# Optimization experiments

Measured on AMD Instinct MI355X. Metric: run time of the kernel, lower is better.

The kernel has to match this reference:

```python
import jax, jax.numpy as jnp
import numpy as np

THRESHOLD = 0.3
NEG_BIG = -2.0 ** 32  # matches tf -2**32 causal mask constant


def setup_inputs() -> dict:
    key = jax.random.key(0)
    kq, kt, kv = jax.random.split(key, 3)
    B, S, D = 16, 2048, 128
    Q = jax.random.normal(kq, (B, S, D), dtype=jnp.float32)
    T = jax.random.normal(kt, (B, S, D), dtype=jnp.float32)
    V = jax.random.normal(kv, (B, S, D), dtype=jnp.float32)
    return {"Q": Q, "T": T, "V": V}


def reference(Q, T, V):
    # scores: [B, S, S]
    A = jnp.einsum('bqd,bkd->bqk', Q, T)
    # Faithful to tf.where(A>thr, A, -2**32 * cast(A>thr)):
    # the false branch evaluates to 0 (mask is 0 there), NOT -2**32.
    A = jnp.where(A > THRESHOLD, A, jnp.zeros((), A.dtype))
    S = Q.shape[1]
    causal = jnp.triu(jnp.ones((S, S), dtype=bool), k=1)  # strictly upper = masked
    A = A + jnp.where(causal, jnp.asarray(NEG_BIG, A.dtype), jnp.zeros((), A.dtype))
    d_k = jnp.asarray(Q.shape[-1], A.dtype)
    A = A / jnp.sqrt(d_k)
    y = jax.nn.softmax(A, axis=-1)
    return jnp.einsum('bqk,bkd->bqd', y, V)
```

## Files before the change

### kernel.cpp

```cpp
#include <hip/hip_runtime.h>
#include <hip/hip_bf16.h>


#define S_LEN 2048
#define D_DIM 128
#define BQ 64
#define BK 64
#define THRESH 0.3f
#define SCALE 0.08838834764831845f

typedef __bf16 bf16x8 __attribute__((ext_vector_type(8)));
typedef float f32x4 __attribute__((ext_vector_type(4)));

__global__ void vt_kernel(const float* __restrict__ V, __bf16* __restrict__ Vt) {
    __shared__ float tile[64][65];
    int bid = blockIdx.x;
    int b  = bid >> 6;
    int t2 = bid & 63;
    int s0 = (t2 >> 1) * 64;
    int d0 = (t2 & 1) * 64;
    int tid = threadIdx.x;
    #pragma unroll
    for (int it = 0; it < 2; ++it) {
        int row = it * 32 + (tid >> 3);
        int c   = (tid & 7) * 8;
        const float* p = V + ((size_t)b * S_LEN + s0 + row) * D_DIM + d0 + c;
        *(f32x4*)(&tile[row][c])     = *(const f32x4*)p;
        *(f32x4*)(&tile[row][c + 4]) = *(const f32x4*)(p + 4);
    }
    __syncthreads();
    #pragma unroll
    for (int it = 0; it < 2; ++it) {
        int dr = it * 32 + (tid >> 3);
        int c  = (tid & 7) * 8;
        bf16x8 w;
        #pragma unroll
        for (int j = 0; j < 8; ++j) w[j] = (__bf16)tile[c + j][dr];
        *(bf16x8*)(Vt + ((size_t)b * D_DIM + d0 + dr) * S_LEN + s0 + c) = w;
    }
}

__global__ __launch_bounds__(256, 2)
void fa_kernel(const float* __restrict__ Q, const float* __restrict__ T,
               const __bf16* __restrict__ Vt, float* __restrict__ O) {
    __shared__ __bf16 Tt[64 * 136];
    __shared__ __bf16 Vl[128 * 72];
    __shared__ __bf16 Pl[4][16 * 72];

    int bid  = blockIdx.x;
    int b    = bid & 15;
    int half = bid >> 8;
    int idx  = (bid >> 4) & 15;
    int qt   = half == 0 ? (31 - idx) : idx;
    int q0   = qt * BQ;

    int tid  = threadIdx.x;
    int lane = tid & 63;
    int wave = tid >> 6;
    int col  = lane & 15;
    int quad = lane >> 4;

    const float* qptr = Q + ((size_t)b * S_LEN + (q0 + wave * 16 + col)) * D_DIM + quad * 8;
    bf16x8 qf[4];
    #pragma unroll
    for (int kk = 0; kk < 4; ++kk) {
        f32x4 a = *(const f32x4*)(qptr + kk * 32);
        f32x4 c = *(const f32x4*)(qptr + kk * 32 + 4);
        #pragma unroll
        for (int j = 0; j < 4; ++j) { qf[kk][j] = (__bf16)a[j]; qf[kk][4 + j] = (__bf16)c[j]; }
    }

    f32x4 oacc[8];
    #pragma unroll
    for (int dt = 0; dt < 8; ++dt) oacc[dt] = {0.f, 0.f, 0.f, 0.f};
    float lsum[4] = {0.f, 0.f, 0.f, 0.f};

    f32x4 tr[8]; bf16x8 vr[4];
    auto loadTiles = [&](int k0) {
        #pragma unroll
        for (int it = 0; it < 4; ++it) {
            int flat = it * 2048 + tid * 8;
            int row = flat >> 7, c = flat & 127;
            const float* p = T + ((size_t)b * S_LEN + k0 + row) * D_DIM + c;
            tr[2 * it]     = *(const f32x4*)p;
            tr[2 * it + 1] = *(const f32x4*)(p + 4);
        }
        #pragma unroll
        for (int it = 0; it < 4; ++it) {
            int flat = it * 2048 + tid * 8;
            int d = flat >> 6, kk2 = flat & 63;
            vr[it] = *(const bf16x8*)(Vt + ((size_t)b * D_DIM + d) * S_LEN + k0 + kk2);
        }
    };
    auto storeTiles = [&]() {
        #pragma unroll
        for (int it = 0; it < 4; ++it) {
            int flat = it * 2048 + tid * 8;
            int row = flat >> 7, c = flat & 127;
            bf16x8 w;
            #pragma unroll
            for (int j = 0; j < 4; ++j) {
                w[j]     = (__bf16)tr[2 * it][j];
                w[4 + j] = (__bf16)tr[2 * it + 1][j];
            }
            *(bf16x8*)(&Tt[row * 136 + c]) = w;
        }
        #pragma unroll
        for (int it = 0; it < 4; ++it) {
            int flat = it * 2048 + tid * 8;
            int d = flat >> 6, kk2 = flat & 63;
            *(bf16x8*)(&Vl[d * 72 + kk2]) = vr[it];
        }
    };

    loadTiles(0);
    storeTiles();
    __syncthreads();

    for (int kt = 0; kt <= qt; ++kt) {
        if (kt < qt) loadTiles((kt + 1) * BK);

        f32x4 sacc[4];
        #pragma unroll
        for (int t = 0; t < 4; ++t) {
            sacc[t] = {0.f, 0.f, 0.f, 0.f};
            #pragma unroll
            for (int kk = 0; kk < 4; ++kk) {
                bf16x8 bf = *(const bf16x8*)(&Tt[(t * 16 + col) * 136 + kk * 32 + quad * 8]);
                sacc[t] = __builtin_amdgcn_mfma_f32_16x16x32_bf16(qf[kk], bf, sacc[t], 0, 0, 0);
            }
        }

        bool diag = (kt == qt);
        float p[4][4];
        #pragma unroll
        for (int t = 0; t < 4; ++t)
            #pragma unroll
            for (int r = 0; r < 4; ++r) {
                float s = sacc[t][r];
                float e = __expf(s * SCALE);
                float w = (s > THRESH) ? e : 1.0f;
                if (diag && (t * 16 + col > wave * 16 + quad * 4 + r)) w = 0.0f;
                p[t][r] = w;
            }
        #pragma unroll
        for (int r = 0; r < 4; ++r)
            lsum[r] += (p[0][r] + p[1][r]) + (p[2][r] + p[3][r]);

        __bf16* pw = &Pl[wave][0];
        #pragma unroll
        for (int t = 0; t < 4; ++t)
            #pragma unroll
            for (int r = 0; r < 4; ++r)
                pw[(quad * 4 + r) * 72 + t * 16 + col] = (__bf16)p[t][r];

        asm volatile("s_waitcnt lgkmcnt(0)" ::: "memory");

        #pragma unroll
        for (int ks = 0; ks < 2; ++ks) {
            bf16x8 af = *(const bf16x8*)(&pw[col * 72 + ks * 32 + quad * 8]);
            #pragma unroll
            for (int dt = 0; dt < 8; ++dt) {
                bf16x8 bf = *(const bf16x8*)(&Vl[(dt * 16 + col) * 72 + ks * 32 + quad * 8]);
                oacc[dt] = __builtin_amdgcn_mfma_f32_16x16x32_bf16(af, bf, oacc[dt], 0, 0, 0);
            }
        }

        __syncthreads();
        if (kt < qt) storeTiles();
        __syncthreads();
    }

    #pragma unroll
    for (int r = 0; r < 4; ++r) {
        float l = lsum[r];
        l += __shfl_xor(l, 1);
        l += __shfl_xor(l, 2);
        l += __shfl_xor(l, 4);
        l += __shfl_xor(l, 8);
        lsum[r] = 1.0f / l;
    }
    float* optr = O + ((size_t)b * S_LEN + q0 + wave * 16) * D_DIM;
    #pragma unroll
    for (int dt = 0; dt < 8; ++dt)
        #pragma unroll
        for (int r = 0; r < 4; ++r)
            optr[(quad * 4 + r) * D_DIM + dt * 16 + col] = oacc[dt][r] * lsum[r];
}

extern "C" void kernel_launch(void* const* d_in, const int* in_sizes, int n_in,
                              void* d_out, int out_size, void* d_ws, size_t ws_size,
                              hipStream_t stream) {
    const float* Q = (const float*)d_in[0];
    const float* T = (const float*)d_in[1];
    const float* V = (const float*)d_in[2];
    __bf16* Vt = (__bf16*)d_ws;
    float* O   = (float*)d_out;

    vt_kernel<<<16 * 64, 256, 0, stream>>>(V, Vt);
    fa_kernel<<<16 * 32, 256, 0, stream>>>(Q, T, Vt, O);
}
```

Baseline: 136.0 us.

## Load K/V fragments directly into registers and pre-cast T to bf16

```diff
diff --git a/kernel.cpp b/kernel.cpp
--- a/kernel.cpp
+++ b/kernel.cpp
@@ -11,6 +11,21 @@
 
 typedef __bf16 bf16x8 __attribute__((ext_vector_type(8)));
 typedef float f32x4 __attribute__((ext_vector_type(4)));
+
+__device__ inline bf16x8 cvt8(const float* p) {
+    f32x4 a = *(const f32x4*)p;
+    f32x4 b = *(const f32x4*)(p + 4);
+    bf16x8 r;
+    #pragma unroll
+    for (int j = 0; j < 4; ++j) { r[j] = (__bf16)a[j]; r[4 + j] = (__bf16)b[j]; }
+    return r;
+}
+
+__global__ void tcast_kernel(const float* __restrict__ T, __bf16* __restrict__ Tb) {
+    size_t i = ((size_t)blockIdx.x * 256 + threadIdx.x) * 16;
+    *(bf16x8*)(Tb + i)     = cvt8(T + i);
+    *(bf16x8*)(Tb + i + 8) = cvt8(T + i + 8);
+}
 
 __global__ void vt_kernel(const float* __restrict__ V, __bf16* __restrict__ Vt) {
     __shared__ float tile[64][65];
@@ -40,11 +55,10 @@
     }
 }
 
+template <bool F32T>
 __global__ __launch_bounds__(256, 2)
-void fa_kernel(const float* __restrict__ Q, const float* __restrict__ T,
+void fa_kernel(const float* __restrict__ Q, const void* __restrict__ Tsrc,
                const __bf16* __restrict__ Vt, float* __restrict__ O) {
-    __shared__ __bf16 Tt[64 * 136];
-    __shared__ __bf16 Vl[128 * 72];
     __shared__ __bf16 Pl[4][16 * 72];
 
     int bid  = blockIdx.x;
@@ -63,73 +77,55 @@
     const float* qptr = Q + ((size_t)b * S_LEN + (q0 + wave * 16 + col)) * D_DIM + quad * 8;
     bf16x8 qf[4];
     #pragma unroll
-    for (int kk = 0; kk < 4; ++kk) {
-        f32x4 a = *(const f32x4*)(qptr + kk * 32);
-        f32x4 c = *(const f32x4*)(qptr + kk * 32 + 4);
-        #pragma unroll
-        for (int j = 0; j < 4; ++j) { qf[kk][j] = (__bf16)a[j]; qf[kk][4 + j] = (__bf16)c[j]; }
-    }
+    for (int kk = 0; kk < 4; ++kk) qf[kk] = cvt8(qptr + kk * 32);
 
     f32x4 oacc[8];
     #pragma unroll
     for (int dt = 0; dt < 8; ++dt) oacc[dt] = {0.f, 0.f, 0.f, 0.f};
     float lsum[4] = {0.f, 0.f, 0.f, 0.f};
 
-    f32x4 tr[8]; bf16x8 vr[4];
-    auto loadTiles = [&](int k0) {
-        #pragma unroll
-        for (int it = 0; it < 4; ++it) {
-            int flat = it * 2048 + tid * 8;
-            int row = flat >> 7, c = flat & 127;
-            const float* p = T + ((size_t)b * S_LEN + k0 + row) * D_DIM + c;
-            tr[2 * it]     = *(const f32x4*)p;
-            tr[2 * it + 1] = *(const f32x4*)(p + 4);
-        }
-        #pragma unroll
-        for (int it = 0; it < 4; ++it) {
-            int flat = it * 2048 + tid * 8;
-            int d = flat >> 6, kk2 = flat & 63;
-            vr[it] = *(const bf16x8*)(Vt + ((size_t)b * D_DIM + d) * S_LEN + k0 + kk2);
-        }
+    const __bf16* Tb   = (const __bf16*)Tsrc;
+    const float*  Tf   = (const float*)Tsrc;
+    const size_t  tbof = (size_t)b * S_LEN * D_DIM;
+    const __bf16* Vb   = Vt + (size_t)b * D_DIM * S_LEN;
+
+    bf16x8 ta[16];
+    bf16x8 vb[16];
+
+    auto loadT = [&](int k0) {
+        #pragma unroll
+        for (int t = 0; t < 4; ++t)
+            #pragma unroll
+            for (int kk = 0; kk < 4; ++kk) {
+                size_t off = tbof + (size_t)(k0 + t * 16 + col) * D_DIM + kk * 32 + quad * 8;
+                if constexpr (F32T) ta[t * 4 + kk] = cvt8(Tf + off);
+                else                ta[t * 4 + kk] = *(const bf16x8*)(Tb + off);
+            }
     };
-    auto storeTiles = [&]() {
-        #pragma unroll
-        for (int it = 0; it < 4; ++it) {
-            int flat = it * 2048 + tid * 8;
-            int row = flat >> 7, c = flat & 127;
-            bf16x8 w;
-            #pragma unroll
-            for (int j = 0; j < 4; ++j) {
-                w[j]     = (__bf16)tr[2 * it][j];
-                w[4 + j] = (__bf16)tr[2 * it + 1][j];
-            }
-            *(bf16x8*)(&Tt[row * 136 + c]) = w;
-        }
-        #pragma unroll
-        for (int it = 0; it < 4; ++it) {
-            int flat = it * 2048 + tid * 8;
-            int d = flat >> 6, kk2 = flat & 63;
-            *(bf16x8*)(&Vl[d * 72 + kk2]) = vr[it];
-        }
+    auto loadV = [&](int k0) {
+        #pragma unroll
+        for (int ks = 0; ks < 2; ++ks)
+            #pragma unroll
+            for (int dt = 0; dt < 8; ++dt)
+                vb[ks * 8 + dt] = *(const bf16x8*)(Vb + (size_t)(dt * 16 + col) * S_LEN
+                                                   + k0 + ks * 32 + quad * 8);
     };
 
-    loadTiles(0);
-    storeTiles();
-    __syncthreads();
+    loadT(0);
+    loadV(0);
 
     for (int kt = 0; kt <= qt; ++kt) {
-        if (kt < qt) loadTiles((kt + 1) * BK);
+        int kn = (kt < qt) ? (kt + 1) * BK : kt * BK;
 
         f32x4 sacc[4];
         #pragma unroll
         for (int t = 0; t < 4; ++t) {
             sacc[t] = {0.f, 0.f, 0.f, 0.f};
             #pragma unroll
-            for (int kk = 0; kk < 4; ++kk) {
-                bf16x8 bf = *(const bf16x8*)(&Tt[(t * 16 + col) * 136 + kk * 32 + quad * 8]);
-                sacc[t] = __builtin_amdgcn_mfma_f32_16x16x32_bf16(qf[kk], bf, sacc[t], 0, 0, 0);
-            }
+            for (int kk = 0; kk < 4; ++kk)
+                sacc[t] = __builtin_amdgcn_mfma_f32_16x16x32_bf16(qf[kk], ta[t * 4 + kk], sacc[t], 0, 0, 0);
         }
+        loadT(kn);
 
         bool diag = (kt == qt);
         float p[4][4];
@@ -160,15 +156,10 @@
         for (int ks = 0; ks < 2; ++ks) {
             bf16x8 af = *(const bf16x8*)(&pw[col * 72 + ks * 32 + quad * 8]);
             #pragma unroll
-            for (int dt = 0; dt < 8; ++dt) {
-                bf16x8 bf = *(const bf16x8*)(&Vl[(dt * 16 + col) * 72 + ks * 32 + quad * 8]);
-                oacc[dt] = __builtin_amdgcn_mfma_f32_16x16x32_bf16(af, bf, oacc[dt], 0, 0, 0);
-            }
+            for (int dt = 0; dt < 8; ++dt)
+                oacc[dt] = __builtin_amdgcn_mfma_f32_16x16x32_bf16(af, vb[ks * 8 + dt], oacc[dt], 0, 0, 0);
         }
-
-        __syncthreads();
-        if (kt < qt) storeTiles();
-        __syncthreads();
+        loadV(kn);
     }
 
     #pragma unroll
@@ -194,9 +185,19 @@
     const float* Q = (const float*)d_in[0];
     const float* T = (const float*)d_in[1];
     const float* V = (const float*)d_in[2];
-    __bf16* Vt = (__bf16*)d_ws;
-    float* O   = (float*)d_out;
-
-    vt_kernel<<<16 * 64, 256, 0, stream>>>(V, Vt);
-    fa_kernel<<<16 * 32, 256, 0, stream>>>(Q, T, Vt, O);
-}
+    float* O = (float*)d_out;
+
+    const size_t HALF = (size_t)16 * 2048 * 128 * sizeof(__bf16);
+
+    if (ws_size >= 2 * HALF) {
+        __bf16* Tb = (__bf16*)d_ws;
+        __bf16* Vt = (__bf16*)((char*)d_ws + HALF);
+        tcast_kernel<<<1024, 256, 0, stream>>>(T, Tb);
+        vt_kernel<<<1024, 256, 0, stream>>>(V, Vt);
+        fa_kernel<false><<<512, 256, 0, stream>>>(Q, Tb, Vt, O);
+    } else {
+        __bf16* Vt = (__bf16*)d_ws;
+        vt_kernel<<<1024, 256, 0, stream>>>(V, Vt);
+        fa_kernel<true><<<512, 256, 0, stream>>>(Q, T, Vt, O);
+    }
+}
```

After: 217.8 us. +60.2%, slower.
